# Performance work log

Hardware: AMD Instinct MI355X
Metric: run time of the kernel (lower is better)

Reference implementation:

```python
import jax, jax.numpy as jnp
import numpy as np

N_NODES = 50000
N_EDGES = 1600000
D_IN = 512
D_OUT = 512


def setup_inputs() -> dict:
    key = jax.random.key(0)
    k1, k2, k3, k4, k5, k6 = jax.random.split(key, 6)
    stdv = 1.0 / np.sqrt(D_OUT)
    x = jax.random.normal(k1, (N_NODES, D_IN), dtype=jnp.float32)
    weight = jax.random.uniform(k2, (D_IN, D_OUT), dtype=jnp.float32, minval=-stdv, maxval=stdv)
    bias = jax.random.uniform(k3, (1, D_OUT), dtype=jnp.float32, minval=-stdv, maxval=stdv)
    edge_val = jax.random.uniform(k4, (N_EDGES,), dtype=jnp.float32)
    edge_row = jax.random.randint(k5, (N_EDGES,), 0, N_NODES, dtype=jnp.int64)
    edge_col = jax.random.randint(k6, (N_EDGES,), 0, N_NODES, dtype=jnp.int64)
    return {"x": x, "weight": weight, "bias": bias,
            "edge_val": edge_val, "edge_row": edge_row, "edge_col": edge_col}


def reference(x, weight, bias, edge_val, edge_row, edge_col):
    # hidden = X @ W  : [N, D_OUT] dense GEMM
    hidden = jnp.matmul(x, weight)
    # spmm: out[i] = sum over edges (i <- j) of adj_val * hidden[j]
    msgs = edge_val[:, None] * hidden[edge_col]            # [E, D_OUT]
    out = jax.ops.segment_sum(msgs, edge_row, num_segments=N_NODES)
    return out + bias
```

## Files before the change

### kernel.cpp

```cpp
#include <hip/hip_runtime.h>

typedef short short8 __attribute__((ext_vector_type(8)));
typedef float v4f   __attribute__((ext_vector_type(4)));

#define N_NODES 50000
#define N_EDGES 1600000
#define DIM     512
#define SCAN_NB 49
#define GNB     2048

__device__ __forceinline__ float bf2f(unsigned short u) {
    unsigned int x = ((unsigned int)u) << 16;
    return __uint_as_float(x);
}
__device__ __forceinline__ unsigned int f2bfu(float f) {
    unsigned int x = __float_as_uint(f);
    unsigned int r = x + 0x7fffu + ((x >> 16) & 1u);
    return r >> 16;
}
__device__ __forceinline__ float lo16(unsigned int u) { return __uint_as_float(u << 16); }
__device__ __forceinline__ float hi16(unsigned int u) { return __uint_as_float(u & 0xffff0000u); }

__device__ __forceinline__ unsigned long long shfl64_xor(unsigned long long v, int m) {
    int lo = (int)(v & 0xffffffffull);
    int hi = (int)(v >> 32);
    lo = __shfl_xor(lo, m);
    hi = __shfl_xor(hi, m);
    return ((unsigned long long)(unsigned int)hi << 32) | (unsigned int)lo;
}

__device__ __forceinline__ void gload_lds16(const void* g, void* l) {
    __builtin_amdgcn_global_load_lds(
        (const __attribute__((address_space(1))) unsigned int*)g,
        (__attribute__((address_space(3))) unsigned int*)l, 16, 0, 0);
}

__global__ void detect_kernel(const unsigned int* __restrict__ xw,
                              const int* __restrict__ erow,
                              int* __restrict__ flags) {
    __shared__ int cbf, cz;
    if (threadIdx.x == 0) { cbf = 0; cz = 0; }
    __syncthreads();
    int lb = 0, lz = 0;
    for (int i = threadIdx.x; i < 1024; i += 256) {
        unsigned int w = xw[i];
        unsigned int e0 = (w >> 7) & 0xFFu;
        unsigned int e1 = (w >> 23) & 0xFFu;
        if (e0 >= 0x70u && e0 <= 0x8Fu && e1 >= 0x70u && e1 <= 0x8Fu) lb++;
        if (erow[2 * i + 1] == 0) lz++;
    }
    atomicAdd(&cbf, lb);
    atomicAdd(&cz, lz);
    __syncthreads();
    if (threadIdx.x == 0) {
        flags[0] = (cbf > 512) ? 1 : 0;
        flags[1] = (cz > 512) ? 1 : 0;
    }
}

__global__ __launch_bounds__(256) void convert_x(const void* __restrict__ Xv,
                                                 unsigned short* __restrict__ Xc,
                                                 const int* __restrict__ flags) {
    if (flags[0] != 0) return;
    const float* Xf = (const float*)Xv;
    size_t i = ((size_t)blockIdx.x * 256 + threadIdx.x) * 8;
    float4 f0 = *(const float4*)(Xf + i);
    float4 f1 = *(const float4*)(Xf + i + 4);
    uint4 o;
    o.x = f2bfu(f0.x) | (f2bfu(f0.y) << 16);
    o.y = f2bfu(f0.z) | (f2bfu(f0.w) << 16);
    o.z = f2bfu(f1.x) | (f2bfu(f1.y) << 16);
    o.w = f2bfu(f1.z) | (f2bfu(f1.w) << 16);
    *(uint4*)(Xc + i) = o;
}

__global__ void transpose_w(const void* __restrict__ Wv,
                            unsigned short* __restrict__ Wt,
                            const int* __restrict__ flags) {
    __shared__ unsigned short tile[32][33];
    const bool fb = flags[0] != 0;
    int bx = blockIdx.x * 32, by = blockIdx.y * 32;
    int tx = threadIdx.x, ty = threadIdx.y;
    if (fb) {
        const unsigned short* W = (const unsigned short*)Wv;
        for (int r = ty; r < 32; r += 8)
            tile[r][tx] = W[(by + r) * DIM + bx + tx];
    } else {
        const float* W = (const float*)Wv;
        for (int r = ty; r < 32; r += 8)
            tile[r][tx] = (unsigned short)f2bfu(W[(by + r) * DIM + bx + tx]);
    }
    __syncthreads();
    for (int r = ty; r < 32; r += 8)
        Wt[(bx + r) * DIM + by + tx] = tile[tx][r];
}

#define TM 128
#define TN 128
#define BK 32

__global__ __launch_bounds__(256) void gemm_kernel(
        const void* __restrict__ Xv,
        const unsigned short* __restrict__ Xc,
        const int have_xc,
        const unsigned short* __restrict__ Wt,
        unsigned short* __restrict__ H,
        const int* __restrict__ flags) {
    __shared__ unsigned short lA[TM * BK];
    __shared__ unsigned short lB[TN * BK];

    const bool fb = flags[0] != 0;
    const bool bfp = fb || (have_xc != 0);
    const unsigned short* Xb = fb ? (const unsigned short*)Xv : Xc;
    const float*          Xf = (const float*)Xv;

    const int t = threadIdx.x;
    const int mBase = blockIdx.y * TM;
    const int nBase = blockIdx.x * TN;
    const int w = t >> 6, lane = t & 63;
    const int lr = lane & 15, quad = lane >> 4;
    const int wr = w >> 1, wc = w & 1;

    v4f acc[4][4];
    #pragma unroll
    for (int i = 0; i < 4; ++i)
        #pragma unroll
        for (int j = 0; j < 4; ++j) acc[i][j] = (v4f)0.0f;

    for (int k0 = 0; k0 < DIM; k0 += BK) {
        #pragma unroll
        for (int r = 0; r < 2; ++r) {
            int chunk = w * 2 + r;
            int row = chunk * 16 + (lane >> 2);
            const unsigned short* gB = Wt + (size_t)(nBase + row) * DIM + k0 + (lane & 3) * 8;
            gload_lds16(gB, lB + chunk * 512);
        }
        if (bfp) {
            #pragma unroll
            for (int r = 0; r < 2; ++r) {
                int chunk = w * 2 + r;
                int row = chunk * 16 + (lane >> 2);
                int grow = mBase + row; if (grow >= N_NODES) grow = N_NODES - 1;
                const unsigned short* gA = Xb + (size_t)grow * DIM + k0 + (lane & 3) * 8;
                gload_lds16(gA, lA + chunk * 512);
            }
        } else {
            #pragma unroll
            for (int rep = 0; rep < 2; ++rep) {
                int idx = rep * 256 + t;
                int r = idx >> 2;
                int cc = (idx & 3) * 8;
                int grow = mBase + r; if (grow >= N_NODES) grow = N_NODES - 1;
                size_t goff = (size_t)grow * DIM + k0 + cc;
                float4 a0 = *(const float4*)(Xf + goff);
                float4 a1 = *(const float4*)(Xf + goff + 4);
                uint4 av;
                av.x = f2bfu(a0.x) | (f2bfu(a0.y) << 16);
                av.y = f2bfu(a0.z) | (f2bfu(a0.w) << 16);
                av.z = f2bfu(a1.x) | (f2bfu(a1.y) << 16);
                av.w = f2bfu(a1.z) | (f2bfu(a1.w) << 16);
                *(uint4*)(&lA[r * BK + cc]) = av;
            }
        }
        __syncthreads();

        short8 bfr[4];
        #pragma unroll
        for (int j = 0; j < 4; ++j)
            bfr[j] = *(const short8*)(&lB[(wc * 64 + j * 16 + lr) * BK + quad * 8]);
        #pragma unroll
        for (int i = 0; i < 4; ++i) {
            short8 a = *(const short8*)(&lA[(wr * 64 + i * 16 + lr) * BK + quad * 8]);
            #pragma unroll
            for (int j = 0; j < 4; ++j)
                acc[i][j] = __builtin_amdgcn_mfma_f32_16x16x32_bf16(a, bfr[j], acc[i][j], 0, 0, 0);
        }
        __syncthreads();
    }

    #pragma unroll
    for (int i = 0; i < 4; ++i) {
        #pragma unroll
        for (int j = 0; j < 4; ++j) {
            #pragma unroll
            for (int r = 0; r < 4; ++r) {
                int gm = mBase + wr * 64 + i * 16 + quad * 4 + r;
                int gn = nBase + wc * 64 + j * 16 + lr;
                if (gm < N_NODES)
                    H[(size_t)gm * DIM + gn] = (unsigned short)f2bfu(acc[i][j][r]);
            }
        }
    }
}

__global__ void hist_kernel(const int* __restrict__ row, int* __restrict__ cnt,
                            const int* __restrict__ flags) {
    const bool f64 = flags[1] != 0;
    int i = blockIdx.x * 256 + threadIdx.x;
    if (i < N_EDGES) {
        int r = f64 ? ((const int2*)row)[i].x : row[i];
        atomicAdd(&cnt[r], 1);
    }
}

__global__ __launch_bounds__(256) void scan1_kernel(const int* __restrict__ cnt,
                                                    int* __restrict__ bsum) {
    __shared__ int sh[256];
    const int b = blockIdx.x, t = threadIdx.x;
    int base = b * 1024 + t * 4;
    int s = 0;
    #pragma unroll
    for (int k = 0; k < 4; ++k) {
        int i = base + k;
        if (i < N_NODES) s += cnt[i];
    }
    sh[t] = s;
    __syncthreads();
    for (int off = 128; off > 0; off >>= 1) {
        if (t < off) sh[t] += sh[t + off];
        __syncthreads();
    }
    if (t == 0) bsum[b] = sh[0];
}

__global__ __launch_bounds__(256) void scan3_kernel(const int* __restrict__ cnt,
                                                    const int* __restrict__ bsum,
                                                    int* __restrict__ start,
                                                    int* __restrict__ cursor) {
    __shared__ int sh[256];
    __shared__ int boffs;
    const int b = blockIdx.x, t = threadIdx.x;
    if (t == 0) {
        int r = 0;
        #pragma unroll 8
        for (int i = 0; i < b; ++i) r += bsum[i];
        boffs = r;
        if (b == 0) start[N_NODES] = N_EDGES;
    }
    int base = b * 1024 + t * 4;
    int v[4];
    #pragma unroll
    for (int k = 0; k < 4; ++k) {
        int i = base + k;
        v[k] = (i < N_NODES) ? cnt[i] : 0;
    }
    int tsum = v[0] + v[1] + v[2] + v[3];
    sh[t] = tsum;
    __syncthreads();
    for (int off = 1; off < 256; off <<= 1) {
        int x = (t >= off) ? sh[t - off] : 0;
        __syncthreads();
        sh[t] += x;
        __syncthreads();
    }
    int excl = sh[t] - tsum + boffs;
    #pragma unroll
    for (int k = 0; k < 4; ++k) {
        int i = base + k;
        if (i < N_NODES) { start[i] = excl; cursor[i] = excl; }
        excl += v[k];
    }
}

__global__ void scatter_kernel(const int* __restrict__ row, const int* __restrict__ col,
                               const void* __restrict__ valv,
                               int* __restrict__ cursor,
                               int2* __restrict__ sCV,
                               const int* __restrict__ flags) {
    const bool fb  = flags[0] != 0;
    const bool f64 = flags[1] != 0;
    int i = blockIdx.x * 256 + threadIdx.x;
    if (i < N_EDGES) {
        int r = f64 ? ((const int2*)row)[i].x : row[i];
        int c = f64 ? ((const int2*)col)[i].x : col[i];
        float v = fb ? bf2f(((const unsigned short*)valv)[i])
                     : ((const float*)valv)[i];
        int p = atomicAdd(&cursor[r], 1);
        int2 cv; cv.x = c; cv.y = __float_as_int(v);
        sCV[p] = cv;
    }
}

__global__ __launch_bounds__(256, 8) void gather_kernel(
        const int* __restrict__ start, const int2* __restrict__ sCV,
        const unsigned short* __restrict__ H,
        const void* __restrict__ biasv, void* __restrict__ outv,
        const int* __restrict__ flags) {
    const bool fb = flags[0] != 0;
    const int lane = threadIdx.x & 63;
    const int wv = threadIdx.x >> 6;

    float b0v = 0, b1v = 0, b2v = 0, b3v = 0, b4v = 0, b5v = 0, b6v = 0, b7v = 0;
    if (fb) {
        uint4 bb = *((const uint4*)biasv + lane);
        b0v = lo16(bb.x); b1v = hi16(bb.x);
        b2v = lo16(bb.y); b3v = hi16(bb.y);
        b4v = lo16(bb.z); b5v = hi16(bb.z);
        b6v = lo16(bb.w); b7v = hi16(bb.w);
    } else {
        const float4* bp = (const float4*)biasv + lane * 2;
        float4 f0 = bp[0], f1 = bp[1];
        b0v = f0.x; b1v = f0.y; b2v = f0.z; b3v = f0.w;
        b4v = f1.x; b5v = f1.y; b6v = f1.z; b7v = f1.w;
    }

    for (int node = blockIdx.x * 4 + wv; node < N_NODES; node += GNB * 4) {
        const int s = start[node], e = start[node + 1];

        float a0 = 0.f, a1 = 0.f, a2 = 0.f, a3 = 0.f;
        float a4 = 0.f, a5 = 0.f, a6 = 0.f, a7 = 0.f;

        for (int p0 = s; p0 < e; p0 += 64) {
            int idx = p0 + lane;
            unsigned long long key;
            if (idx < e) {
                int2 cv = sCV[idx];
                key = ((unsigned long long)(unsigned int)cv.x << 32) | (unsigned int)cv.y;
            } else {
                key = ~0ull;
            }
            #pragma unroll
            for (int k = 2; k <= 64; k <<= 1) {
                #pragma unroll
                for (int j = k >> 1; j > 0; j >>= 1) {
                    unsigned long long other = shfl64_xor(key, j);
                    bool keep_min = (((lane & j) == 0) == ((lane & k) == 0));
                    unsigned long long mn = (key < other) ? key : other;
                    unsigned long long mx = (key < other) ? other : key;
                    key = keep_min ? mn : mx;
                }
            }
            int cnt = e - p0; if (cnt > 64) cnt = 64;
            int klo = (int)(key & 0xffffffffull);
            int khi = (int)(key >> 32);
            #pragma unroll 4
            for (int q = 0; q < cnt; ++q) {
                int col  = __builtin_amdgcn_readlane(khi, q);
                float v  = __int_as_float(__builtin_amdgcn_readlane(klo, q));
                uint4 h = *((const uint4*)(H + ((size_t)(unsigned int)col << 9)) + lane);
                a0 = fmaf(v, lo16(h.x), a0);
                a1 = fmaf(v, hi16(h.x), a1);
                a2 = fmaf(v, lo16(h.y), a2);
                a3 = fmaf(v, hi16(h.y), a3);
                a4 = fmaf(v, lo16(h.z), a4);
                a5 = fmaf(v, hi16(h.z), a5);
                a6 = fmaf(v, lo16(h.w), a6);
                a7 = fmaf(v, hi16(h.w), a7);
            }
        }

        if (fb) {
            uint4 o;
            o.x = f2bfu(a0 + b0v) | (f2bfu(a1 + b1v) << 16);
            o.y = f2bfu(a2 + b2v) | (f2bfu(a3 + b3v) << 16);
            o.z = f2bfu(a4 + b4v) | (f2bfu(a5 + b5v) << 16);
            o.w = f2bfu(a6 + b6v) | (f2bfu(a7 + b7v) << 16);
            *((uint4*)((unsigned short*)outv + (size_t)node * DIM) + lane) = o;
        } else {
            float4 o0, o1;
            o0.x = a0 + b0v; o0.y = a1 + b1v; o0.z = a2 + b2v; o0.w = a3 + b3v;
            o1.x = a4 + b4v; o1.y = a5 + b5v; o1.z = a6 + b6v; o1.w = a7 + b7v;
            float4* op = (float4*)((float*)outv + (size_t)node * DIM) + lane * 2;
            op[0] = o0; op[1] = o1;
        }
    }
}

extern "C" void kernel_launch(void* const* d_in, const int* in_sizes, int n_in,
                              void* d_out, int out_size, void* d_ws, size_t ws_size,
                              hipStream_t stream) {
    const void* X    = d_in[0];
    const void* W    = d_in[1];
    const void* bias = d_in[2];
    const void* eval = d_in[3];
    const int*  erow = (const int*)d_in[4];
    const int*  ecol = (const int*)d_in[5];

    char* w = (char*)d_ws;
    size_t o = 0;
    int* flags = (int*)(w + o); o += 256;
    unsigned short* hidden = (unsigned short*)(w + o); o += (size_t)N_NODES * DIM * 2;
    int2*  sCV    = (int2*)(w + o);  o += (size_t)N_EDGES * 8;
    int*   cnt    = (int*)(w + o);   o += 200704;
    int*   start  = (int*)(w + o);   o += 200704;
    int*   cursor = (int*)(w + o);   o += 200704;
    unsigned short* Wt = (unsigned short*)(w + o); o += (size_t)DIM * DIM * 2;
    int*   bsum   = (int*)(w + o);   o += 256;
    size_t base_end = o;
    unsigned short* Xc = (unsigned short*)(w + o);
    size_t need_xc = base_end + (size_t)N_NODES * DIM * 2;
    const int have_xc = (ws_size >= need_xc) ? 1 : 0;

    hipMemsetAsync(cnt, 0, N_NODES * sizeof(int), stream);

    detect_kernel<<<1, 256, 0, stream>>>((const unsigned int*)X, erow, flags);
    if (have_xc)
        convert_x<<<(N_NODES * DIM) / (256 * 8), 256, 0, stream>>>(X, Xc, flags);
    transpose_w<<<dim3(16, 16), dim3(32, 8), 0, stream>>>(W, Wt, flags);
    gemm_kernel<<<dim3(DIM / TN, (N_NODES + TM - 1) / TM), 256, 0, stream>>>(
        X, Xc, have_xc, Wt, hidden, flags);
    hist_kernel<<<(N_EDGES + 255) / 256, 256, 0, stream>>>(erow, cnt, flags);
    scan1_kernel<<<SCAN_NB, 256, 0, stream>>>(cnt, bsum);
    scan3_kernel<<<SCAN_NB, 256, 0, stream>>>(cnt, bsum, start, cursor);
    scatter_kernel<<<(N_EDGES + 255) / 256, 256, 0, stream>>>(erow, ecol, eval, cursor, sCV, flags);
    gather_kernel<<<GNB, 256, 0, stream>>>(start, sCV, hidden, bias, d_out, flags);
}
```

Measured before the change: 672.5 us.

## Bucket edges by column block and wave, gather in two column-half passes

Edges are now binned by (column block of 4096 nodes, wave, row group), so each wave owns 13 output rows and walks the source columns block by block. The idea is that all waves read hidden rows from the same column region at roughly the same time, which improves L2/cache reuse of H. The gather is split into two passes over the feature dimension, each lane handling 4 features, with 13 row accumulators kept in registers. In exchange the histogram and scan now run over about 692K keys instead of 50K, a separate block-offset scan kernel is added, and each H access is only 8 bytes per lane, so there are more load instructions.

Measured after the change: 779.3 us. +15.9%, slower.

```diff
diff --git a/kernel.cpp b/kernel.cpp
--- a/kernel.cpp
+++ b/kernel.cpp
@@ -6,8 +6,11 @@
 #define N_NODES 50000
 #define N_EDGES 1600000
 #define DIM     512
-#define SCAN_NB 49
-#define GNB     2048
+#define NCB     13
+#define NWAVE   4096
+#define NK      13
+#define NKEYS   692224
+#define SCAN_NB 676
 
 __device__ __forceinline__ float bf2f(unsigned short u) {
     unsigned int x = ((unsigned int)u) << 16;
@@ -21,12 +24,8 @@
 __device__ __forceinline__ float lo16(unsigned int u) { return __uint_as_float(u << 16); }
 __device__ __forceinline__ float hi16(unsigned int u) { return __uint_as_float(u & 0xffff0000u); }
 
-__device__ __forceinline__ unsigned long long shfl64_xor(unsigned long long v, int m) {
-    int lo = (int)(v & 0xffffffffull);
-    int hi = (int)(v >> 32);
-    lo = __shfl_xor(lo, m);
-    hi = __shfl_xor(hi, m);
-    return ((unsigned long long)(unsigned int)hi << 32) | (unsigned int)lo;
+__device__ __forceinline__ int edge_key(int r, int c) {
+    return (c >> 12) * (NWAVE * NK) + (r & (NWAVE - 1)) * NK + (r >> 12);
 }
 
 __device__ __forceinline__ void gload_lds16(const void* g, void* l) {
@@ -193,13 +192,15 @@
     }
 }
 
-__global__ void hist_kernel(const int* __restrict__ row, int* __restrict__ cnt,
+__global__ void hist_kernel(const int* __restrict__ row, const int* __restrict__ col,
+                            int* __restrict__ cnt,
                             const int* __restrict__ flags) {
     const bool f64 = flags[1] != 0;
     int i = blockIdx.x * 256 + threadIdx.x;
     if (i < N_EDGES) {
         int r = f64 ? ((const int2*)row)[i].x : row[i];
-        atomicAdd(&cnt[r], 1);
+        int c = f64 ? ((const int2*)col)[i].x : col[i];
+        atomicAdd(&cnt[edge_key(r, c)], 1);
     }
 }
 
@@ -212,7 +213,7 @@
     #pragma unroll
     for (int k = 0; k < 4; ++k) {
         int i = base + k;
-        if (i < N_NODES) s += cnt[i];
+        if (i < NKEYS) s += cnt[i];
     }
     sh[t] = s;
     __syncthreads();
@@ -221,6 +222,28 @@
         __syncthreads();
     }
     if (t == 0) bsum[b] = sh[0];
+}
+
+__global__ __launch_bounds__(256) void scan2_kernel(int* __restrict__ bsum) {
+    __shared__ int sh[256];
+    const int t = threadIdx.x;
+    int i0 = t * 3;
+    int v0 = (i0     < SCAN_NB) ? bsum[i0]     : 0;
+    int v1 = (i0 + 1 < SCAN_NB) ? bsum[i0 + 1] : 0;
+    int v2 = (i0 + 2 < SCAN_NB) ? bsum[i0 + 2] : 0;
+    int s = v0 + v1 + v2;
+    sh[t] = s;
+    __syncthreads();
+    for (int off = 1; off < 256; off <<= 1) {
+        int x = (t >= off) ? sh[t - off] : 0;
+        __syncthreads();
+        sh[t] += x;
+        __syncthreads();
+    }
+    int excl = sh[t] - s;
+    if (i0     < SCAN_NB) bsum[i0]     = excl;
+    if (i0 + 1 < SCAN_NB) bsum[i0 + 1] = excl + v0;
+    if (i0 + 2 < SCAN_NB) bsum[i0 + 2] = excl + v0 + v1;
 }
 
 __global__ __launch_bounds__(256) void scan3_kernel(const int* __restrict__ cnt,
@@ -228,21 +251,15 @@
                                                     int* __restrict__ start,
                                                     int* __restrict__ cursor) {
     __shared__ int sh[256];
-    __shared__ int boffs;
     const int b = blockIdx.x, t = threadIdx.x;
-    if (t == 0) {
-        int r = 0;
-        #pragma unroll 8
-        for (int i = 0; i < b; ++i) r += bsum[i];
-        boffs = r;
-        if (b == 0) start[N_NODES] = N_EDGES;
-    }
+    if (b == 0 && t == 0) start[NKEYS] = N_EDGES;
+    int boffs = bsum[b];
     int base = b * 1024 + t * 4;
     int v[4];
     #pragma unroll
     for (int k = 0; k < 4; ++k) {
         int i = base + k;
-        v[k] = (i < N_NODES) ? cnt[i] : 0;
+        v[k] = (i < NKEYS) ? cnt[i] : 0;
     }
     int tsum = v[0] + v[1] + v[2] + v[3];
     sh[t] = tsum;
@@ -257,7 +274,7 @@
     #pragma unroll
     for (int k = 0; k < 4; ++k) {
         int i = base + k;
-        if (i < N_NODES) { start[i] = excl; cursor[i] = excl; }
+        if (i < NKEYS) { start[i] = excl; cursor[i] = excl; }
         excl += v[k];
     }
 }
@@ -275,93 +292,80 @@
         int c = f64 ? ((const int2*)col)[i].x : col[i];
         float v = fb ? bf2f(((const unsigned short*)valv)[i])
                      : ((const float*)valv)[i];
-        int p = atomicAdd(&cursor[r], 1);
+        int p = atomicAdd(&cursor[edge_key(r, c)], 1);
         int2 cv; cv.x = c; cv.y = __float_as_int(v);
         sCV[p] = cv;
     }
 }
 
-__global__ __launch_bounds__(256, 8) void gather_kernel(
+__global__ __launch_bounds__(256, 4) void gather_kernel(
         const int* __restrict__ start, const int2* __restrict__ sCV,
         const unsigned short* __restrict__ H,
         const void* __restrict__ biasv, void* __restrict__ outv,
-        const int* __restrict__ flags) {
+        const int* __restrict__ flags, const int pass) {
     const bool fb = flags[0] != 0;
     const int lane = threadIdx.x & 63;
-    const int wv = threadIdx.x >> 6;
-
-    float b0v = 0, b1v = 0, b2v = 0, b3v = 0, b4v = 0, b5v = 0, b6v = 0, b7v = 0;
-    if (fb) {
-        uint4 bb = *((const uint4*)biasv + lane);
-        b0v = lo16(bb.x); b1v = hi16(bb.x);
-        b2v = lo16(bb.y); b3v = hi16(bb.y);
-        b4v = lo16(bb.z); b5v = hi16(bb.z);
-        b6v = lo16(bb.w); b7v = hi16(bb.w);
-    } else {
-        const float4* bp = (const float4*)biasv + lane * 2;
-        float4 f0 = bp[0], f1 = bp[1];
-        b0v = f0.x; b1v = f0.y; b2v = f0.z; b3v = f0.w;
-        b4v = f1.x; b5v = f1.y; b6v = f1.z; b7v = f1.w;
-    }
-
-    for (int node = blockIdx.x * 4 + wv; node < N_NODES; node += GNB * 4) {
-        const int s = start[node], e = start[node + 1];
-
-        float a0 = 0.f, a1 = 0.f, a2 = 0.f, a3 = 0.f;
-        float a4 = 0.f, a5 = 0.f, a6 = 0.f, a7 = 0.f;
-
-        for (int p0 = s; p0 < e; p0 += 64) {
-            int idx = p0 + lane;
-            unsigned long long key;
-            if (idx < e) {
-                int2 cv = sCV[idx];
-                key = ((unsigned long long)(unsigned int)cv.x << 32) | (unsigned int)cv.y;
-            } else {
-                key = ~0ull;
-            }
+    const int w = blockIdx.x * 4 + (threadIdx.x >> 6);
+    const int d0 = pass * 256 + lane * 4;
+
+    float acc[NK][4];
+    #pragma unroll
+    for (int k = 0; k < NK; ++k)
+        #pragma unroll
+        for (int j = 0; j < 4; ++j) acc[k][j] = 0.f;
+
+    for (int cb = 0; cb < NCB; ++cb) {
+        int rbase = cb * (NWAVE * NK) + w * NK;
+        int b[NK + 1];
+        #pragma unroll
+        for (int i = 0; i <= NK; ++i) b[i] = start[rbase + i];
+        int runs = b[0], rune = b[NK];
+
+        for (int q0 = runs; q0 < rune; q0 += 64) {
+            int idx = q0 + lane;
+            int clamped = (idx < rune) ? idx : (rune - 1);
+            int2 cv = sCV[clamped];
+            int qe = (rune < q0 + 64) ? rune : (q0 + 64);
             #pragma unroll
-            for (int k = 2; k <= 64; k <<= 1) {
-                #pragma unroll
-                for (int j = k >> 1; j > 0; j >>= 1) {
-                    unsigned long long other = shfl64_xor(key, j);
-                    bool keep_min = (((lane & j) == 0) == ((lane & k) == 0));
-                    unsigned long long mn = (key < other) ? key : other;
-                    unsigned long long mx = (key < other) ? other : key;
-                    key = keep_min ? mn : mx;
+            for (int k = 0; k < NK; ++k) {
+                int lo = (b[k] > q0) ? b[k] : q0;
+                int hi = (b[k + 1] < qe) ? b[k + 1] : qe;
+                for (int q = lo; q < hi; ++q) {
+                    int col = __builtin_amdgcn_readlane(cv.x, q - q0);
+                    float v = __int_as_float(__builtin_amdgcn_readlane(cv.y, q - q0));
+                    uint2 h = *(const uint2*)(H + (size_t)col * DIM + d0);
+                    acc[k][0] = fmaf(v, lo16(h.x), acc[k][0]);
+                    acc[k][1] = fmaf(v, hi16(h.x), acc[k][1]);
+                    acc[k][2] = fmaf(v, lo16(h.y), acc[k][2]);
+                    acc[k][3] = fmaf(v, hi16(h.y), acc[k][3]);
                 }
             }
-            int cnt = e - p0; if (cnt > 64) cnt = 64;
-            int klo = (int)(key & 0xffffffffull);
-            int khi = (int)(key >> 32);
-            #pragma unroll 4
-            for (int q = 0; q < cnt; ++q) {
-                int col  = __builtin_amdgcn_readlane(khi, q);
-                float v  = __int_as_float(__builtin_amdgcn_readlane(klo, q));
-                uint4 h = *((const uint4*)(H + ((size_t)(unsigned int)col << 9)) + lane);
-                a0 = fmaf(v, lo16(h.x), a0);
-                a1 = fmaf(v, hi16(h.x), a1);
-                a2 = fmaf(v, lo16(h.y), a2);
-                a3 = fmaf(v, hi16(h.y), a3);
-                a4 = fmaf(v, lo16(h.z), a4);
-                a5 = fmaf(v, hi16(h.z), a5);
-                a6 = fmaf(v, lo16(h.w), a6);
-                a7 = fmaf(v, hi16(h.w), a7);
-            }
-        }
-
+        }
+        __syncthreads();
+    }
+
+    float b0, b1, b2, b3;
+    if (fb) {
+        uint2 bb = *(const uint2*)((const unsigned short*)biasv + d0);
+        b0 = lo16(bb.x); b1 = hi16(bb.x); b2 = lo16(bb.y); b3 = hi16(bb.y);
+    } else {
+        const float* bp = (const float*)biasv + d0;
+        b0 = bp[0]; b1 = bp[1]; b2 = bp[2]; b3 = bp[3];
+    }
+    #pragma unroll
+    for (int k = 0; k < NK; ++k) {
+        int node = w + k * NWAVE;
+        if (node >= N_NODES) break;
         if (fb) {
-            uint4 o;
-            o.x = f2bfu(a0 + b0v) | (f2bfu(a1 + b1v) << 16);
-            o.y = f2bfu(a2 + b2v) | (f2bfu(a3 + b3v) << 16);
-            o.z = f2bfu(a4 + b4v) | (f2bfu(a5 + b5v) << 16);
-            o.w = f2bfu(a6 + b6v) | (f2bfu(a7 + b7v) << 16);
-            *((uint4*)((unsigned short*)outv + (size_t)node * DIM) + lane) = o;
+            uint2 o;
+            o.x = f2bfu(acc[k][0] + b0) | (f2bfu(acc[k][1] + b1) << 16);
+            o.y = f2bfu(acc[k][2] + b2) | (f2bfu(acc[k][3] + b3) << 16);
+            *(uint2*)((unsigned short*)outv + (size_t)node * DIM + d0) = o;
         } else {
-            float4 o0, o1;
-            o0.x = a0 + b0v; o0.y = a1 + b1v; o0.z = a2 + b2v; o0.w = a3 + b3v;
-            o1.x = a4 + b4v; o1.y = a5 + b5v; o1.z = a6 + b6v; o1.w = a7 + b7v;
-            float4* op = (float4*)((float*)outv + (size_t)node * DIM) + lane * 2;
-            op[0] = o0; op[1] = o1;
+            float4 o;
+            o.x = acc[k][0] + b0; o.y = acc[k][1] + b1;
+            o.z = acc[k][2] + b2; o.w = acc[k][3] + b3;
+            *(float4*)((float*)outv + (size_t)node * DIM + d0) = o;
         }
     }
 }
@@ -381,17 +385,17 @@
     int* flags = (int*)(w + o); o += 256;
     unsigned short* hidden = (unsigned short*)(w + o); o += (size_t)N_NODES * DIM * 2;
     int2*  sCV    = (int2*)(w + o);  o += (size_t)N_EDGES * 8;
-    int*   cnt    = (int*)(w + o);   o += 200704;
-    int*   start  = (int*)(w + o);   o += 200704;
-    int*   cursor = (int*)(w + o);   o += 200704;
+    int*   cnt    = (int*)(w + o);   o += 2769152;
+    int*   start  = (int*)(w + o);   o += 2769152;
+    int*   cursor = (int*)(w + o);   o += 2769152;
     unsigned short* Wt = (unsigned short*)(w + o); o += (size_t)DIM * DIM * 2;
-    int*   bsum   = (int*)(w + o);   o += 256;
+    int*   bsum   = (int*)(w + o);   o += 4096;
     size_t base_end = o;
     unsigned short* Xc = (unsigned short*)(w + o);
     size_t need_xc = base_end + (size_t)N_NODES * DIM * 2;
     const int have_xc = (ws_size >= need_xc) ? 1 : 0;
 
-    hipMemsetAsync(cnt, 0, N_NODES * sizeof(int), stream);
+    hipMemsetAsync(cnt, 0, (size_t)NKEYS * sizeof(int), stream);
 
     detect_kernel<<<1, 256, 0, stream>>>((const unsigned int*)X, erow, flags);
     if (have_xc)
@@ -399,9 +403,11 @@
     transpose_w<<<dim3(16, 16), dim3(32, 8), 0, stream>>>(W, Wt, flags);
     gemm_kernel<<<dim3(DIM / TN, (N_NODES + TM - 1) / TM), 256, 0, stream>>>(
         X, Xc, have_xc, Wt, hidden, flags);
-    hist_kernel<<<(N_EDGES + 255) / 256, 256, 0, stream>>>(erow, cnt, flags);
+    hist_kernel<<<(N_EDGES + 255) / 256, 256, 0, stream>>>(erow, ecol, cnt, flags);
     scan1_kernel<<<SCAN_NB, 256, 0, stream>>>(cnt, bsum);
+    scan2_kernel<<<1, 256, 0, stream>>>(bsum);
     scan3_kernel<<<SCAN_NB, 256, 0, stream>>>(cnt, bsum, start, cursor);
     scatter_kernel<<<(N_EDGES + 255) / 256, 256, 0, stream>>>(erow, ecol, eval, cursor, sCV, flags);
-    gather_kernel<<<GNB, 256, 0, stream>>>(start, sCV, hidden, bias, d_out, flags);
-}
+    gather_kernel<<<1024, 256, 0, stream>>>(start, sCV, hidden, bias, d_out, flags, 0);
+    gather_kernel<<<1024, 256, 0, stream>>>(start, sCV, hidden, bias, d_out, flags, 1);
+}
```
